# Optimization experiments

Hardware: AMD Instinct MI355X
Metric: run time of the kernel (lower is better)

Reference implementation:

```python
import jax, jax.numpy as jnp
import numpy as np

ROUTING_ITERS = 3
EPS = 1e-8


def squash(x):
    # scale = ||x||^2 / (1 + ||x||^2); out = scale * x / (||x|| + eps)
    norm = jnp.linalg.norm(x, axis=-1, keepdims=True)
    scale = norm ** 2 / (1.0 + norm ** 2)
    return scale * x / (norm + EPS)


def setup_inputs() -> dict:
    key = jax.random.key(0)
    kx, kw = jax.random.split(key)
    B, R, C, IC, OC = 256, 1152, 10, 8, 16
    x = jax.random.normal(kx, (B, R, IC), dtype=jnp.float32)
    # learned prediction weights: [1, num_routes, num_capsules, in_ch, out_ch]
    weights = jax.random.normal(kw, (1, R, C, IC, OC), dtype=jnp.float32)
    return {"x": x, "weights": weights}


def reference(x, weights):
    # prediction vectors u_hat[b,r,c,o] = sum_i x[b,r,i] * W[r,c,i,o]
    u = jnp.einsum('bri,rcio->brco', x, weights[0])  # [B,R,C,OC]
    b = jnp.zeros(u.shape[:3], dtype=u.dtype)        # routing logits [B,R,C]
    v = jnp.zeros(u.shape[:1] + u.shape[2:], dtype=u.dtype)
    for _ in range(ROUTING_ITERS):
        c = jax.nn.softmax(b, axis=-1)               # coupling coeffs over capsules
        s = jnp.einsum('brc,brco->bco', c, u)        # weighted sum over routes
        v = squash(s)                                # [B,C,OC]
        b = b + jnp.einsum('brco,bco->brc', u, v)    # agreement update
    return v
```

## Files before the change

### kernel.cpp

```cpp
#include <hip/hip_runtime.h>
#include <cstdint>
#include <cstddef>

#define NB 256
#define NR 1152
#define NC 10
#define NI 8
#define NO 16
#define NSPLIT 6
#define RSPL 192

static __device__ __forceinline__ uint32_t bf16_pack2(float lo, float hi) {
    uint32_t vl = __float_as_uint(lo);
    vl = vl + 0x7FFFu + ((vl >> 16) & 1u);
    uint32_t vh = __float_as_uint(hi);
    vh = vh + 0x7FFFu + ((vh >> 16) & 1u);
    return (vl >> 16) | (vh & 0xFFFF0000u);
}

__global__ __launch_bounds__(320, 2) void caps_u_kernel(
    const float* __restrict__ x, const float* __restrict__ W,
    uint32_t* __restrict__ u)
{
    const int t  = threadIdx.x;
    const int c  = t >> 5;
    const int rl = (t & 31) >> 2;
    const int oq = t & 3;
    const int rc = blockIdx.x >> 4;
    const int bg = blockIdx.x & 15;
    const int b0 = bg * 16;
    const int r  = rc * 8 + rl;

    __shared__ float xs[16][8][8];

    if (t < 256) {
        const int bi = t >> 4, rem = t & 15;
        const int rr = rem >> 1, hf = rem & 1;
        *(float4*)&xs[bi][rr][hf * 4] =
            *(const float4*)(x + ((size_t)(b0 + bi) * NR + rc * 8 + rr) * 8 + hf * 4);
    }

    const float* wb = W + ((size_t)r * NC + c) * (NI * NO) + oq * 4;
    float4 wf[8];
#pragma unroll
    for (int i = 0; i < 8; ++i) wf[i] = *(const float4*)(wb + i * NO);

    __syncthreads();

    for (int bi = 0; bi < 16; ++bi) {
        float xr[8];
#pragma unroll
        for (int i = 0; i < 8; ++i) xr[i] = xs[bi][rl][i];
        float ax = 0.f, ay = 0.f, az = 0.f, aw = 0.f;
#pragma unroll
        for (int i = 0; i < 8; ++i) {
            const float xv = xr[i];
            ax = fmaf(xv, wf[i].x, ax); ay = fmaf(xv, wf[i].y, ay);
            az = fmaf(xv, wf[i].z, az); aw = fmaf(xv, wf[i].w, aw);
        }
        uint2 s;
        s.x = bf16_pack2(ax, ay);
        s.y = bf16_pack2(az, aw);
        *(uint2*)(u + (((size_t)(b0 + bi) * NC + c) * NR + r) * 8 + oq * 2) = s;
    }
}

__global__ __launch_bounds__(256, 2) void caps_pass_kernel(
    const uint32_t* __restrict__ u, const float* __restrict__ vsum,
    float* __restrict__ part, const int mode)
{
    const int b  = blockIdx.x / NSPLIT;
    const int sp = blockIdx.x % NSPLIT;
    const int t  = threadIdx.x;
    const int oq = t & 3;
    const int rl = t >> 2;

    __shared__ float vss[160];
    __shared__ float sred[4][160];

    if (mode != 0 && t < 160) vss[t] = vsum[(size_t)b * 160 + t];
    __syncthreads();

    float acc[10][4];
#pragma unroll
    for (int c = 0; c < 10; ++c)
#pragma unroll
        for (int j = 0; j < 4; ++j) acc[c][j] = 0.f;

    const uint2* ub = (const uint2*)u + (size_t)b * NC * NR * 4 + oq;

    for (int k = 0; k < 3; ++k) {
        const int r = sp * RSPL + k * 64 + rl;
        uint2 q[10];
#pragma unroll
        for (int c = 0; c < 10; ++c) q[c] = ub[((size_t)c * NR + r) * 4];

        if (mode != 0) {
            float lg[10];
#pragma unroll
            for (int c = 0; c < 10; ++c) {
                const float4 vq = *(const float4*)&vss[c * 16 + oq * 4];
                float d = __uint_as_float(q[c].x << 16) * vq.x;
                d = fmaf(__uint_as_float(q[c].x & 0xFFFF0000u), vq.y, d);
                d = fmaf(__uint_as_float(q[c].y << 16),         vq.z, d);
                d = fmaf(__uint_as_float(q[c].y & 0xFFFF0000u), vq.w, d);
                lg[c] = d;
            }
#pragma unroll
            for (int c = 0; c < 10; ++c) {
                lg[c] += __shfl_xor(lg[c], 1);
                lg[c] += __shfl_xor(lg[c], 2);
            }
            float m = lg[0];
#pragma unroll
            for (int c = 1; c < 10; ++c) m = fmaxf(m, lg[c]);
            float wgt[10], ssum = 0.f;
#pragma unroll
            for (int c = 0; c < 10; ++c) { wgt[c] = __expf(lg[c] - m); ssum += wgt[c]; }
            const float inv = 1.f / ssum;
#pragma unroll
            for (int c = 0; c < 10; ++c) {
                const float wv = wgt[c] * inv;
                acc[c][0] = fmaf(wv, __uint_as_float(q[c].x << 16),         acc[c][0]);
                acc[c][1] = fmaf(wv, __uint_as_float(q[c].x & 0xFFFF0000u), acc[c][1]);
                acc[c][2] = fmaf(wv, __uint_as_float(q[c].y << 16),         acc[c][2]);
                acc[c][3] = fmaf(wv, __uint_as_float(q[c].y & 0xFFFF0000u), acc[c][3]);
            }
        } else {
#pragma unroll
            for (int c = 0; c < 10; ++c) {
                acc[c][0] += __uint_as_float(q[c].x << 16);
                acc[c][1] += __uint_as_float(q[c].x & 0xFFFF0000u);
                acc[c][2] += __uint_as_float(q[c].y << 16);
                acc[c][3] += __uint_as_float(q[c].y & 0xFFFF0000u);
            }
        }
    }

#pragma unroll
    for (int off = 4; off <= 32; off <<= 1)
#pragma unroll
        for (int c = 0; c < 10; ++c)
#pragma unroll
            for (int j = 0; j < 4; ++j) acc[c][j] += __shfl_xor(acc[c][j], off);

    const int wv = t >> 6;
    if ((t & 63) < 4) {
#pragma unroll
        for (int c = 0; c < 10; ++c)
#pragma unroll
            for (int j = 0; j < 4; ++j)
                sred[wv][c * 16 + oq * 4 + j] = acc[c][j];
    }
    __syncthreads();

    if (t < 160) {
        float s = sred[0][t] + sred[1][t] + sred[2][t] + sred[3][t];
        if (mode == 0) s *= 0.1f;
        part[((size_t)sp * NB + b) * 160 + t] = s;
    }
}

__global__ __launch_bounds__(192) void caps_reduce_kernel(
    const float* __restrict__ part, float* __restrict__ vsum,
    float* __restrict__ out, const int mode)
{
    const int b = blockIdx.x;
    const int t = threadIdx.x;
    if (t >= 160) return;
    float s = 0.f;
#pragma unroll
    for (int sp = 0; sp < NSPLIT; ++sp)
        s += part[((size_t)sp * NB + b) * 160 + t];
    float n2 = s * s;
    n2 += __shfl_xor(n2, 1);
    n2 += __shfl_xor(n2, 2);
    n2 += __shfl_xor(n2, 4);
    n2 += __shfl_xor(n2, 8);
    const float nrm   = sqrtf(n2);
    const float scale = n2 / (1.f + n2) / (nrm + 1e-8f);
    const float v = scale * s;
    if (mode == 0)      vsum[(size_t)b * 160 + t] = v;
    else if (mode == 1) vsum[(size_t)b * 160 + t] += v;
    else                out[(size_t)b * 160 + t] = v;
}

extern "C" void kernel_launch(void* const* d_in, const int* in_sizes, int n_in,
                              void* d_out, int out_size, void* d_ws, size_t ws_size,
                              hipStream_t stream) {
    const float* x = (const float*)d_in[0];
    const float* W = (const float*)d_in[1];
    float* out = (float*)d_out;

    uint8_t*  ws  = (uint8_t*)d_ws;
    uint32_t* u   = (uint32_t*)ws;
    float*    prt = (float*)(ws + 94371840u);
    float*    vsm = (float*)(ws + 94371840u + 983040u);

    caps_u_kernel     <<<2304, 320, 0, stream>>>(x, W, u);
    caps_pass_kernel  <<<NB * NSPLIT, 256, 0, stream>>>(u, vsm, prt, 0);
    caps_reduce_kernel<<<NB, 192, 0, stream>>>(prt, vsm, nullptr, 0);
    caps_pass_kernel  <<<NB * NSPLIT, 256, 0, stream>>>(u, vsm, prt, 1);
    caps_reduce_kernel<<<NB, 192, 0, stream>>>(prt, vsm, nullptr, 1);
    caps_pass_kernel  <<<NB * NSPLIT, 256, 0, stream>>>(u, vsm, prt, 1);
    caps_reduce_kernel<<<NB, 192, 0, stream>>>(prt, nullptr, out, 2);
}
```

Measured before the change: 159.4 us.

## Compute first routing pass from fp32 x and W instead of rereading u

Adds a separate kernel that recomputes the prediction vectors from x and W and reduces them across routes within each block, writing per-route-chunk partial sums. A dedicated reduce kernel turns these into the first squash output. This replaces the first full read of the bf16 u tensor, and the first pass now uses exact fp32 rather than bf16. The routing pass kernels now use a finer route split (18 splits of 64 routes, one route per thread), trading more blocks and a larger partial-sum buffer for higher parallelism. The cost is an extra read of W and a recompute of the einsum, plus a 23 MB partial buffer that the reduce kernel must read.

```diff
diff --git a/kernel.cpp b/kernel.cpp
--- a/kernel.cpp
+++ b/kernel.cpp
@@ -7,8 +7,9 @@
 #define NC 10
 #define NI 8
 #define NO 16
-#define NSPLIT 6
-#define RSPL 192
+#define NSPLIT 18
+#define RSPL 64
+#define NRC 144
 
 static __device__ __forceinline__ uint32_t bf16_pack2(float lo, float hi) {
     uint32_t vl = __float_as_uint(lo);
@@ -65,76 +66,136 @@
     }
 }
 
+__global__ __launch_bounds__(320, 2) void caps_s1_kernel(
+    const float* __restrict__ x, const float* __restrict__ W,
+    float* __restrict__ part1)
+{
+    const int t  = threadIdx.x;
+    const int c  = t >> 5;
+    const int rl = (t & 31) >> 2;
+    const int oq = t & 3;
+    const int rc = blockIdx.x >> 4;
+    const int bg = blockIdx.x & 15;
+    const int b0 = bg * 16;
+    const int r  = rc * 8 + rl;
+
+    __shared__ float xs[16][8][8];
+
+    if (t < 256) {
+        const int bi = t >> 4, rem = t & 15;
+        const int rr = rem >> 1, hf = rem & 1;
+        *(float4*)&xs[bi][rr][hf * 4] =
+            *(const float4*)(x + ((size_t)(b0 + bi) * NR + rc * 8 + rr) * 8 + hf * 4);
+    }
+
+    const float* wb = W + ((size_t)r * NC + c) * (NI * NO) + oq * 4;
+    float4 wf[8];
+#pragma unroll
+    for (int i = 0; i < 8; ++i) wf[i] = *(const float4*)(wb + i * NO);
+
+    __syncthreads();
+
+    for (int bi = 0; bi < 16; ++bi) {
+        float xr[8];
+#pragma unroll
+        for (int i = 0; i < 8; ++i) xr[i] = xs[bi][rl][i];
+        float a[4] = {0.f, 0.f, 0.f, 0.f};
+#pragma unroll
+        for (int i = 0; i < 8; ++i) {
+            const float xv = xr[i];
+            a[0] = fmaf(xv, wf[i].x, a[0]); a[1] = fmaf(xv, wf[i].y, a[1]);
+            a[2] = fmaf(xv, wf[i].z, a[2]); a[3] = fmaf(xv, wf[i].w, a[3]);
+        }
+#pragma unroll
+        for (int off = 4; off <= 16; off <<= 1)
+#pragma unroll
+            for (int j = 0; j < 4; ++j) a[j] += __shfl_xor(a[j], off);
+        if ((t & 28) == 0) {
+            *(float4*)(part1 + ((size_t)rc * NB + b0 + bi) * 160 + c * 16 + oq * 4)
+                = *(float4*)a;
+        }
+    }
+}
+
+__global__ __launch_bounds__(192) void caps_s1_reduce_kernel(
+    const float* __restrict__ part1, float* __restrict__ vsum)
+{
+    const int b = blockIdx.x;
+    const int t = threadIdx.x;
+    if (t >= 160) return;
+    float s0 = 0.f, s1 = 0.f, s2 = 0.f, s3 = 0.f;
+    const float* p = part1 + (size_t)b * 160 + t;
+#pragma unroll 4
+    for (int g = 0; g < NRC; g += 4) {
+        s0 += p[(size_t)(g + 0) * NB * 160];
+        s1 += p[(size_t)(g + 1) * NB * 160];
+        s2 += p[(size_t)(g + 2) * NB * 160];
+        s3 += p[(size_t)(g + 3) * NB * 160];
+    }
+    const float s = 0.1f * ((s0 + s1) + (s2 + s3));
+    float n2 = s * s;
+    n2 += __shfl_xor(n2, 1);
+    n2 += __shfl_xor(n2, 2);
+    n2 += __shfl_xor(n2, 4);
+    n2 += __shfl_xor(n2, 8);
+    const float nrm   = sqrtf(n2);
+    const float scale = n2 / (1.f + n2) / (nrm + 1e-8f);
+    vsum[(size_t)b * 160 + t] = scale * s;
+}
+
 __global__ __launch_bounds__(256, 2) void caps_pass_kernel(
     const uint32_t* __restrict__ u, const float* __restrict__ vsum,
-    float* __restrict__ part, const int mode)
+    float* __restrict__ part2)
 {
     const int b  = blockIdx.x / NSPLIT;
     const int sp = blockIdx.x % NSPLIT;
     const int t  = threadIdx.x;
     const int oq = t & 3;
     const int rl = t >> 2;
+    const int r  = sp * RSPL + rl;
 
     __shared__ float vss[160];
     __shared__ float sred[4][160];
 
-    if (mode != 0 && t < 160) vss[t] = vsum[(size_t)b * 160 + t];
-    __syncthreads();
+    if (t < 160) vss[t] = vsum[(size_t)b * 160 + t];
+    __syncthreads();
+
+    const uint2* ub = (const uint2*)u + (size_t)b * NC * NR * 4 + oq;
+    uint2 q[10];
+#pragma unroll
+    for (int c = 0; c < 10; ++c) q[c] = ub[((size_t)c * NR + r) * 4];
+
+    float lg[10];
+#pragma unroll
+    for (int c = 0; c < 10; ++c) {
+        const float4 vq = *(const float4*)&vss[c * 16 + oq * 4];
+        float d = __uint_as_float(q[c].x << 16) * vq.x;
+        d = fmaf(__uint_as_float(q[c].x & 0xFFFF0000u), vq.y, d);
+        d = fmaf(__uint_as_float(q[c].y << 16),         vq.z, d);
+        d = fmaf(__uint_as_float(q[c].y & 0xFFFF0000u), vq.w, d);
+        lg[c] = d;
+    }
+#pragma unroll
+    for (int c = 0; c < 10; ++c) {
+        lg[c] += __shfl_xor(lg[c], 1);
+        lg[c] += __shfl_xor(lg[c], 2);
+    }
+    float m = lg[0];
+#pragma unroll
+    for (int c = 1; c < 10; ++c) m = fmaxf(m, lg[c]);
+    float wgt[10], ssum = 0.f;
+#pragma unroll
+    for (int c = 0; c < 10; ++c) { wgt[c] = __expf(lg[c] - m); ssum += wgt[c]; }
+    const float inv = 1.f / ssum;
 
     float acc[10][4];
 #pragma unroll
-    for (int c = 0; c < 10; ++c)
-#pragma unroll
-        for (int j = 0; j < 4; ++j) acc[c][j] = 0.f;
-
-    const uint2* ub = (const uint2*)u + (size_t)b * NC * NR * 4 + oq;
-
-    for (int k = 0; k < 3; ++k) {
-        const int r = sp * RSPL + k * 64 + rl;
-        uint2 q[10];
-#pragma unroll
-        for (int c = 0; c < 10; ++c) q[c] = ub[((size_t)c * NR + r) * 4];
-
-        if (mode != 0) {
-            float lg[10];
-#pragma unroll
-            for (int c = 0; c < 10; ++c) {
-                const float4 vq = *(const float4*)&vss[c * 16 + oq * 4];
-                float d = __uint_as_float(q[c].x << 16) * vq.x;
-                d = fmaf(__uint_as_float(q[c].x & 0xFFFF0000u), vq.y, d);
-                d = fmaf(__uint_as_float(q[c].y << 16),         vq.z, d);
-                d = fmaf(__uint_as_float(q[c].y & 0xFFFF0000u), vq.w, d);
-                lg[c] = d;
-            }
-#pragma unroll
-            for (int c = 0; c < 10; ++c) {
-                lg[c] += __shfl_xor(lg[c], 1);
-                lg[c] += __shfl_xor(lg[c], 2);
-            }
-            float m = lg[0];
-#pragma unroll
-            for (int c = 1; c < 10; ++c) m = fmaxf(m, lg[c]);
-            float wgt[10], ssum = 0.f;
-#pragma unroll
-            for (int c = 0; c < 10; ++c) { wgt[c] = __expf(lg[c] - m); ssum += wgt[c]; }
-            const float inv = 1.f / ssum;
-#pragma unroll
-            for (int c = 0; c < 10; ++c) {
-                const float wv = wgt[c] * inv;
-                acc[c][0] = fmaf(wv, __uint_as_float(q[c].x << 16),         acc[c][0]);
-                acc[c][1] = fmaf(wv, __uint_as_float(q[c].x & 0xFFFF0000u), acc[c][1]);
-                acc[c][2] = fmaf(wv, __uint_as_float(q[c].y << 16),         acc[c][2]);
-                acc[c][3] = fmaf(wv, __uint_as_float(q[c].y & 0xFFFF0000u), acc[c][3]);
-            }
-        } else {
-#pragma unroll
-            for (int c = 0; c < 10; ++c) {
-                acc[c][0] += __uint_as_float(q[c].x << 16);
-                acc[c][1] += __uint_as_float(q[c].x & 0xFFFF0000u);
-                acc[c][2] += __uint_as_float(q[c].y << 16);
-                acc[c][3] += __uint_as_float(q[c].y & 0xFFFF0000u);
-            }
-        }
+    for (int c = 0; c < 10; ++c) {
+        const float wv = wgt[c] * inv;
+        acc[c][0] = wv * __uint_as_float(q[c].x << 16);
+        acc[c][1] = wv * __uint_as_float(q[c].x & 0xFFFF0000u);
+        acc[c][2] = wv * __uint_as_float(q[c].y << 16);
+        acc[c][3] = wv * __uint_as_float(q[c].y & 0xFFFF0000u);
     }
 
 #pragma unroll
@@ -155,14 +216,13 @@
     __syncthreads();
 
     if (t < 160) {
-        float s = sred[0][t] + sred[1][t] + sred[2][t] + sred[3][t];
-        if (mode == 0) s *= 0.1f;
-        part[((size_t)sp * NB + b) * 160 + t] = s;
+        part2[((size_t)sp * NB + b) * 160 + t]
+            = sred[0][t] + sred[1][t] + sred[2][t] + sred[3][t];
     }
 }
 
 __global__ __launch_bounds__(192) void caps_reduce_kernel(
-    const float* __restrict__ part, float* __restrict__ vsum,
+    const float* __restrict__ part2, float* __restrict__ vsum,
     float* __restrict__ out, const int mode)
 {
     const int b = blockIdx.x;
@@ -171,7 +231,7 @@
     float s = 0.f;
 #pragma unroll
     for (int sp = 0; sp < NSPLIT; ++sp)
-        s += part[((size_t)sp * NB + b) * 160 + t];
+        s += part2[((size_t)sp * NB + b) * 160 + t];
     float n2 = s * s;
     n2 += __shfl_xor(n2, 1);
     n2 += __shfl_xor(n2, 2);
@@ -180,9 +240,8 @@
     const float nrm   = sqrtf(n2);
     const float scale = n2 / (1.f + n2) / (nrm + 1e-8f);
     const float v = scale * s;
-    if (mode == 0)      vsum[(size_t)b * 160 + t] = v;
-    else if (mode == 1) vsum[(size_t)b * 160 + t] += v;
-    else                out[(size_t)b * 160 + t] = v;
+    if (mode == 1) vsum[(size_t)b * 160 + t] += v;
+    else           out[(size_t)b * 160 + t] = v;
 }
 
 extern "C" void kernel_launch(void* const* d_in, const int* in_sizes, int n_in,
@@ -192,16 +251,17 @@
     const float* W = (const float*)d_in[1];
     float* out = (float*)d_out;
 
-    uint8_t*  ws  = (uint8_t*)d_ws;
-    uint32_t* u   = (uint32_t*)ws;
-    float*    prt = (float*)(ws + 94371840u);
-    float*    vsm = (float*)(ws + 94371840u + 983040u);
-
-    caps_u_kernel     <<<2304, 320, 0, stream>>>(x, W, u);
-    caps_pass_kernel  <<<NB * NSPLIT, 256, 0, stream>>>(u, vsm, prt, 0);
-    caps_reduce_kernel<<<NB, 192, 0, stream>>>(prt, vsm, nullptr, 0);
-    caps_pass_kernel  <<<NB * NSPLIT, 256, 0, stream>>>(u, vsm, prt, 1);
-    caps_reduce_kernel<<<NB, 192, 0, stream>>>(prt, vsm, nullptr, 1);
-    caps_pass_kernel  <<<NB * NSPLIT, 256, 0, stream>>>(u, vsm, prt, 1);
-    caps_reduce_kernel<<<NB, 192, 0, stream>>>(prt, nullptr, out, 2);
-}
+    uint8_t*  ws   = (uint8_t*)d_ws;
+    uint32_t* u    = (uint32_t*)ws;
+    float*    prt1 = (float*)(ws + 94371840u);
+    float*    prt2 = (float*)(ws + 94371840u + 23592960u);
+    float*    vsm  = (float*)(ws + 94371840u + 23592960u + 2949120u);
+
+    caps_u_kernel        <<<2304, 320, 0, stream>>>(x, W, u);
+    caps_s1_kernel       <<<2304, 320, 0, stream>>>(x, W, prt1);
+    caps_s1_reduce_kernel<<<NB, 192, 0, stream>>>(prt1, vsm);
+    caps_pass_kernel     <<<NB * NSPLIT, 256, 0, stream>>>(u, vsm, prt2);
+    caps_reduce_kernel   <<<NB, 192, 0, stream>>>(prt2, vsm, nullptr, 1);
+    caps_pass_kernel     <<<NB * NSPLIT, 256, 0, stream>>>(u, vsm, prt2);
+    caps_reduce_kernel   <<<NB, 192, 0, stream>>>(prt2, nullptr, out, 2);
+}
```

Result: slower. 227.4 us (+42.7%).

## Split routing passes finer, preload all u loads, shorten shuffle reduction

Applied to the files above, without the earlier changes.

The route dimension is now split 9 ways instead of 6, giving more blocks. Each thread issues both halves of its u loads up front so more memory requests are in flight, and the pass kernel's launch bound is raised to 4 blocks per CU. The cross-lane shuffle reduction stops at offset 8, and the rest of the sum goes through a larger shared-memory table, trading shuffles for LDS traffic. The u kernel reads x from LDS as float4 and drops its occupancy hint; the partial buffer grows and the vsum offset moves to match.

```diff
diff --git a/kernel.cpp b/kernel.cpp
--- a/kernel.cpp
+++ b/kernel.cpp
@@ -7,8 +7,8 @@
 #define NC 10
 #define NI 8
 #define NO 16
-#define NSPLIT 6
-#define RSPL 192
+#define NSPLIT 9
+#define RSPL 128
 
 static __device__ __forceinline__ uint32_t bf16_pack2(float lo, float hi) {
     uint32_t vl = __float_as_uint(lo);
@@ -18,7 +18,7 @@
     return (vl >> 16) | (vh & 0xFFFF0000u);
 }
 
-__global__ __launch_bounds__(320, 2) void caps_u_kernel(
+__global__ __launch_bounds__(320) void caps_u_kernel(
     const float* __restrict__ x, const float* __restrict__ W,
     uint32_t* __restrict__ u)
 {
@@ -48,9 +48,10 @@
     __syncthreads();
 
     for (int bi = 0; bi < 16; ++bi) {
-        float xr[8];
-#pragma unroll
-        for (int i = 0; i < 8; ++i) xr[i] = xs[bi][rl][i];
+        const float4 xv4a = *(const float4*)&xs[bi][rl][0];
+        const float4 xv4b = *(const float4*)&xs[bi][rl][4];
+        const float xr[8] = {xv4a.x, xv4a.y, xv4a.z, xv4a.w,
+                             xv4b.x, xv4b.y, xv4b.z, xv4b.w};
         float ax = 0.f, ay = 0.f, az = 0.f, aw = 0.f;
 #pragma unroll
         for (int i = 0; i < 8; ++i) {
@@ -65,7 +66,7 @@
     }
 }
 
-__global__ __launch_bounds__(256, 2) void caps_pass_kernel(
+__global__ __launch_bounds__(256, 4) void caps_pass_kernel(
     const uint32_t* __restrict__ u, const float* __restrict__ vsum,
     float* __restrict__ part, const int mode)
 {
@@ -74,36 +75,39 @@
     const int t  = threadIdx.x;
     const int oq = t & 3;
     const int rl = t >> 2;
+    const int r0 = sp * RSPL + rl;
 
     __shared__ float vss[160];
-    __shared__ float sred[4][160];
+    __shared__ float sred[16][164];
 
     if (mode != 0 && t < 160) vss[t] = vsum[(size_t)b * 160 + t];
     __syncthreads();
 
+    const uint2* ub = (const uint2*)u + (size_t)b * NC * NR * 4 + oq;
+
+    uint2 q[2][10];
+#pragma unroll
+    for (int c = 0; c < 10; ++c) q[0][c] = ub[((size_t)c * NR + r0) * 4];
+#pragma unroll
+    for (int c = 0; c < 10; ++c) q[1][c] = ub[((size_t)c * NR + r0 + 64) * 4];
+
     float acc[10][4];
 #pragma unroll
     for (int c = 0; c < 10; ++c)
 #pragma unroll
         for (int j = 0; j < 4; ++j) acc[c][j] = 0.f;
 
-    const uint2* ub = (const uint2*)u + (size_t)b * NC * NR * 4 + oq;
-
-    for (int k = 0; k < 3; ++k) {
-        const int r = sp * RSPL + k * 64 + rl;
-        uint2 q[10];
-#pragma unroll
-        for (int c = 0; c < 10; ++c) q[c] = ub[((size_t)c * NR + r) * 4];
-
+#pragma unroll
+    for (int h = 0; h < 2; ++h) {
         if (mode != 0) {
             float lg[10];
 #pragma unroll
             for (int c = 0; c < 10; ++c) {
                 const float4 vq = *(const float4*)&vss[c * 16 + oq * 4];
-                float d = __uint_as_float(q[c].x << 16) * vq.x;
-                d = fmaf(__uint_as_float(q[c].x & 0xFFFF0000u), vq.y, d);
-                d = fmaf(__uint_as_float(q[c].y << 16),         vq.z, d);
-                d = fmaf(__uint_as_float(q[c].y & 0xFFFF0000u), vq.w, d);
+                float d = __uint_as_float(q[h][c].x << 16) * vq.x;
+                d = fmaf(__uint_as_float(q[h][c].x & 0xFFFF0000u), vq.y, d);
+                d = fmaf(__uint_as_float(q[h][c].y << 16),         vq.z, d);
+                d = fmaf(__uint_as_float(q[h][c].y & 0xFFFF0000u), vq.w, d);
                 lg[c] = d;
             }
 #pragma unroll
@@ -121,41 +125,45 @@
 #pragma unroll
             for (int c = 0; c < 10; ++c) {
                 const float wv = wgt[c] * inv;
-                acc[c][0] = fmaf(wv, __uint_as_float(q[c].x << 16),         acc[c][0]);
-                acc[c][1] = fmaf(wv, __uint_as_float(q[c].x & 0xFFFF0000u), acc[c][1]);
-                acc[c][2] = fmaf(wv, __uint_as_float(q[c].y << 16),         acc[c][2]);
-                acc[c][3] = fmaf(wv, __uint_as_float(q[c].y & 0xFFFF0000u), acc[c][3]);
+                acc[c][0] = fmaf(wv, __uint_as_float(q[h][c].x << 16),         acc[c][0]);
+                acc[c][1] = fmaf(wv, __uint_as_float(q[h][c].x & 0xFFFF0000u), acc[c][1]);
+                acc[c][2] = fmaf(wv, __uint_as_float(q[h][c].y << 16),         acc[c][2]);
+                acc[c][3] = fmaf(wv, __uint_as_float(q[h][c].y & 0xFFFF0000u), acc[c][3]);
             }
         } else {
 #pragma unroll
             for (int c = 0; c < 10; ++c) {
-                acc[c][0] += __uint_as_float(q[c].x << 16);
-                acc[c][1] += __uint_as_float(q[c].x & 0xFFFF0000u);
-                acc[c][2] += __uint_as_float(q[c].y << 16);
-                acc[c][3] += __uint_as_float(q[c].y & 0xFFFF0000u);
+                acc[c][0] += __uint_as_float(q[h][c].x << 16);
+                acc[c][1] += __uint_as_float(q[h][c].x & 0xFFFF0000u);
+                acc[c][2] += __uint_as_float(q[h][c].y << 16);
+                acc[c][3] += __uint_as_float(q[h][c].y & 0xFFFF0000u);
             }
         }
     }
 
 #pragma unroll
-    for (int off = 4; off <= 32; off <<= 1)
+    for (int off = 4; off <= 8; off <<= 1)
 #pragma unroll
         for (int c = 0; c < 10; ++c)
 #pragma unroll
             for (int j = 0; j < 4; ++j) acc[c][j] += __shfl_xor(acc[c][j], off);
 
-    const int wv = t >> 6;
-    if ((t & 63) < 4) {
+    const int lane = t & 63;
+    const int wv   = t >> 6;
+    const int g    = lane >> 4;
+    if (((lane >> 2) & 3) == 0) {
 #pragma unroll
         for (int c = 0; c < 10; ++c)
 #pragma unroll
             for (int j = 0; j < 4; ++j)
-                sred[wv][c * 16 + oq * 4 + j] = acc[c][j];
+                sred[wv * 4 + g][c * 16 + oq * 4 + j] = acc[c][j];
     }
     __syncthreads();
 
     if (t < 160) {
-        float s = sred[0][t] + sred[1][t] + sred[2][t] + sred[3][t];
+        float s = 0.f;
+#pragma unroll
+        for (int w = 0; w < 16; ++w) s += sred[w][t];
         if (mode == 0) s *= 0.1f;
         part[((size_t)sp * NB + b) * 160 + t] = s;
     }
@@ -195,7 +203,7 @@
     uint8_t*  ws  = (uint8_t*)d_ws;
     uint32_t* u   = (uint32_t*)ws;
     float*    prt = (float*)(ws + 94371840u);
-    float*    vsm = (float*)(ws + 94371840u + 983040u);
+    float*    vsm = (float*)(ws + 94371840u + 1474560u);
 
     caps_u_kernel     <<<2304, 320, 0, stream>>>(x, W, u);
     caps_pass_kernel  <<<NB * NSPLIT, 256, 0, stream>>>(u, vsm, prt, 0);
```

Measured after the change: 199.8 us. +25.4%, slower.

## Widen per-thread work to 8 outputs with 16-byte loads and halve route splits

Applied to the files above, without the earlier changes.

Both the prediction kernel and the routing pass kernel now give each thread 8 output channels instead of 4. Stores and loads of the bf16 u tensor become 16-byte vectors, and the prediction kernel handles 16 routes per block. The pass kernel uses 3 route splits of 384 instead of 6 of 192, so it writes fewer partials and sums them in a 32-row shared-memory reduction. The aim is fewer, wider memory transactions on the bandwidth-bound u reads and writes. The cost is higher register pressure and fewer blocks in the pass kernel, which may reduce occupancy.

```diff
diff --git a/kernel.cpp b/kernel.cpp
--- a/kernel.cpp
+++ b/kernel.cpp
@@ -7,8 +7,8 @@
 #define NC 10
 #define NI 8
 #define NO 16
-#define NSPLIT 6
-#define RSPL 192
+#define NSPLIT 3
+#define RSPL 384
 
 static __device__ __forceinline__ uint32_t bf16_pack2(float lo, float hi) {
     uint32_t vl = __float_as_uint(lo);
@@ -24,44 +24,51 @@
 {
     const int t  = threadIdx.x;
     const int c  = t >> 5;
-    const int rl = (t & 31) >> 2;
-    const int oq = t & 3;
+    const int rl = (t & 31) >> 1;
+    const int oh = t & 1;
     const int rc = blockIdx.x >> 4;
     const int bg = blockIdx.x & 15;
     const int b0 = bg * 16;
-    const int r  = rc * 8 + rl;
-
-    __shared__ float xs[16][8][8];
-
-    if (t < 256) {
-        const int bi = t >> 4, rem = t & 15;
+    const int r  = rc * 16 + rl;
+
+    __shared__ float xs[16][16][12];
+
+    for (int k = t; k < 512; k += 320) {
+        const int bi = k >> 5, rem = k & 31;
         const int rr = rem >> 1, hf = rem & 1;
         *(float4*)&xs[bi][rr][hf * 4] =
-            *(const float4*)(x + ((size_t)(b0 + bi) * NR + rc * 8 + rr) * 8 + hf * 4);
-    }
-
-    const float* wb = W + ((size_t)r * NC + c) * (NI * NO) + oq * 4;
-    float4 wf[8];
-#pragma unroll
-    for (int i = 0; i < 8; ++i) wf[i] = *(const float4*)(wb + i * NO);
-
+            *(const float4*)(x + ((size_t)(b0 + bi) * NR + rc * 16 + rr) * 8 + hf * 4);
+    }
+
+    const float* wb = W + ((size_t)r * NC + c) * (NI * NO) + oh * 8;
+    float4 wf[16];
+#pragma unroll
+    for (int i = 0; i < 8; ++i) {
+        wf[i * 2 + 0] = *(const float4*)(wb + i * NO);
+        wf[i * 2 + 1] = *(const float4*)(wb + i * NO + 4);
+    }
     __syncthreads();
 
     for (int bi = 0; bi < 16; ++bi) {
-        float xr[8];
-#pragma unroll
-        for (int i = 0; i < 8; ++i) xr[i] = xs[bi][rl][i];
-        float ax = 0.f, ay = 0.f, az = 0.f, aw = 0.f;
+        const float4 xa = *(const float4*)&xs[bi][rl][0];
+        const float4 xb = *(const float4*)&xs[bi][rl][4];
+        const float xr[8] = {xa.x, xa.y, xa.z, xa.w, xb.x, xb.y, xb.z, xb.w};
+        float a[8];
+#pragma unroll
+        for (int j = 0; j < 8; ++j) a[j] = 0.f;
 #pragma unroll
         for (int i = 0; i < 8; ++i) {
             const float xv = xr[i];
-            ax = fmaf(xv, wf[i].x, ax); ay = fmaf(xv, wf[i].y, ay);
-            az = fmaf(xv, wf[i].z, az); aw = fmaf(xv, wf[i].w, aw);
-        }
-        uint2 s;
-        s.x = bf16_pack2(ax, ay);
-        s.y = bf16_pack2(az, aw);
-        *(uint2*)(u + (((size_t)(b0 + bi) * NC + c) * NR + r) * 8 + oq * 2) = s;
+            const float4 w0 = wf[i * 2 + 0], w1 = wf[i * 2 + 1];
+            a[0] = fmaf(xv, w0.x, a[0]); a[1] = fmaf(xv, w0.y, a[1]);
+            a[2] = fmaf(xv, w0.z, a[2]); a[3] = fmaf(xv, w0.w, a[3]);
+            a[4] = fmaf(xv, w1.x, a[4]); a[5] = fmaf(xv, w1.y, a[5]);
+            a[6] = fmaf(xv, w1.z, a[6]); a[7] = fmaf(xv, w1.w, a[7]);
+        }
+        uint4 s;
+        s.x = bf16_pack2(a[0], a[1]); s.y = bf16_pack2(a[2], a[3]);
+        s.z = bf16_pack2(a[4], a[5]); s.w = bf16_pack2(a[6], a[7]);
+        *(uint4*)(u + (((size_t)(b0 + bi) * NC + c) * NR + r) * 8 + oh * 4) = s;
     }
 }
 
@@ -72,90 +79,101 @@
     const int b  = blockIdx.x / NSPLIT;
     const int sp = blockIdx.x % NSPLIT;
     const int t  = threadIdx.x;
-    const int oq = t & 3;
-    const int rl = t >> 2;
+    const int oh = t & 1;
+    const int rl = t >> 1;
 
     __shared__ float vss[160];
-    __shared__ float sred[4][160];
+    __shared__ float sred[32][164];
 
     if (mode != 0 && t < 160) vss[t] = vsum[(size_t)b * 160 + t];
     __syncthreads();
 
-    float acc[10][4];
+    float acc[10][8];
 #pragma unroll
     for (int c = 0; c < 10; ++c)
 #pragma unroll
-        for (int j = 0; j < 4; ++j) acc[c][j] = 0.f;
-
-    const uint2* ub = (const uint2*)u + (size_t)b * NC * NR * 4 + oq;
+        for (int j = 0; j < 8; ++j) acc[c][j] = 0.f;
+
+    const uint4* ub = (const uint4*)u + (size_t)b * NC * NR * 2 + oh;
 
     for (int k = 0; k < 3; ++k) {
-        const int r = sp * RSPL + k * 64 + rl;
-        uint2 q[10];
-#pragma unroll
-        for (int c = 0; c < 10; ++c) q[c] = ub[((size_t)c * NR + r) * 4];
-
+        const int r = sp * RSPL + k * 128 + rl;
+        uint4 q[10];
+#pragma unroll
+        for (int c = 0; c < 10; ++c) q[c] = ub[((size_t)c * NR + r) * 2];
+
+        float wgt[10];
         if (mode != 0) {
             float lg[10];
 #pragma unroll
             for (int c = 0; c < 10; ++c) {
-                const float4 vq = *(const float4*)&vss[c * 16 + oq * 4];
-                float d = __uint_as_float(q[c].x << 16) * vq.x;
-                d = fmaf(__uint_as_float(q[c].x & 0xFFFF0000u), vq.y, d);
-                d = fmaf(__uint_as_float(q[c].y << 16),         vq.z, d);
-                d = fmaf(__uint_as_float(q[c].y & 0xFFFF0000u), vq.w, d);
+                const float4 v0 = *(const float4*)&vss[c * 16 + oh * 8];
+                const float4 v1 = *(const float4*)&vss[c * 16 + oh * 8 + 4];
+                float d;
+                d = __uint_as_float(q[c].x << 16)                 * v0.x;
+                d = fmaf(__uint_as_float(q[c].x & 0xFFFF0000u), v0.y, d);
+                d = fmaf(__uint_as_float(q[c].y << 16),         v0.z, d);
+                d = fmaf(__uint_as_float(q[c].y & 0xFFFF0000u), v0.w, d);
+                d = fmaf(__uint_as_float(q[c].z << 16),         v1.x, d);
+                d = fmaf(__uint_as_float(q[c].z & 0xFFFF0000u), v1.y, d);
+                d = fmaf(__uint_as_float(q[c].w << 16),         v1.z, d);
+                d = fmaf(__uint_as_float(q[c].w & 0xFFFF0000u), v1.w, d);
                 lg[c] = d;
             }
 #pragma unroll
-            for (int c = 0; c < 10; ++c) {
+            for (int c = 0; c < 10; ++c)
                 lg[c] += __shfl_xor(lg[c], 1);
-                lg[c] += __shfl_xor(lg[c], 2);
-            }
             float m = lg[0];
 #pragma unroll
             for (int c = 1; c < 10; ++c) m = fmaxf(m, lg[c]);
-            float wgt[10], ssum = 0.f;
+            float ssum = 0.f;
 #pragma unroll
             for (int c = 0; c < 10; ++c) { wgt[c] = __expf(lg[c] - m); ssum += wgt[c]; }
             const float inv = 1.f / ssum;
 #pragma unroll
-            for (int c = 0; c < 10; ++c) {
-                const float wv = wgt[c] * inv;
-                acc[c][0] = fmaf(wv, __uint_as_float(q[c].x << 16),         acc[c][0]);
-                acc[c][1] = fmaf(wv, __uint_as_float(q[c].x & 0xFFFF0000u), acc[c][1]);
-                acc[c][2] = fmaf(wv, __uint_as_float(q[c].y << 16),         acc[c][2]);
-                acc[c][3] = fmaf(wv, __uint_as_float(q[c].y & 0xFFFF0000u), acc[c][3]);
-            }
+            for (int c = 0; c < 10; ++c) wgt[c] *= inv;
         } else {
 #pragma unroll
-            for (int c = 0; c < 10; ++c) {
-                acc[c][0] += __uint_as_float(q[c].x << 16);
-                acc[c][1] += __uint_as_float(q[c].x & 0xFFFF0000u);
-                acc[c][2] += __uint_as_float(q[c].y << 16);
-                acc[c][3] += __uint_as_float(q[c].y & 0xFFFF0000u);
-            }
-        }
-    }
-
-#pragma unroll
-    for (int off = 4; off <= 32; off <<= 1)
+            for (int c = 0; c < 10; ++c) wgt[c] = 1.f;
+        }
+#pragma unroll
+        for (int c = 0; c < 10; ++c) {
+            const float wv = wgt[c];
+            acc[c][0] = fmaf(wv, __uint_as_float(q[c].x << 16),         acc[c][0]);
+            acc[c][1] = fmaf(wv, __uint_as_float(q[c].x & 0xFFFF0000u), acc[c][1]);
+            acc[c][2] = fmaf(wv, __uint_as_float(q[c].y << 16),         acc[c][2]);
+            acc[c][3] = fmaf(wv, __uint_as_float(q[c].y & 0xFFFF0000u), acc[c][3]);
+            acc[c][4] = fmaf(wv, __uint_as_float(q[c].z << 16),         acc[c][4]);
+            acc[c][5] = fmaf(wv, __uint_as_float(q[c].z & 0xFFFF0000u), acc[c][5]);
+            acc[c][6] = fmaf(wv, __uint_as_float(q[c].w << 16),         acc[c][6]);
+            acc[c][7] = fmaf(wv, __uint_as_float(q[c].w & 0xFFFF0000u), acc[c][7]);
+        }
+    }
+
+#pragma unroll
+    for (int off = 2; off <= 4; off <<= 1)
 #pragma unroll
         for (int c = 0; c < 10; ++c)
 #pragma unroll
-            for (int j = 0; j < 4; ++j) acc[c][j] += __shfl_xor(acc[c][j], off);
-
-    const int wv = t >> 6;
-    if ((t & 63) < 4) {
-#pragma unroll
-        for (int c = 0; c < 10; ++c)
-#pragma unroll
-            for (int j = 0; j < 4; ++j)
-                sred[wv][c * 16 + oq * 4 + j] = acc[c][j];
+            for (int j = 0; j < 8; ++j) acc[c][j] += __shfl_xor(acc[c][j], off);
+
+    const int lane = t & 63;
+    const int wv   = t >> 6;
+    if (((lane >> 1) & 3) == 0) {
+        const int g   = lane >> 3;
+        const int row = wv * 8 + g;
+#pragma unroll
+        for (int c = 0; c < 10; ++c) {
+            *(float4*)&sred[row][c * 16 + oh * 8]     = *(float4*)&acc[c][0];
+            *(float4*)&sred[row][c * 16 + oh * 8 + 4] = *(float4*)&acc[c][4];
+        }
     }
     __syncthreads();
 
     if (t < 160) {
-        float s = sred[0][t] + sred[1][t] + sred[2][t] + sred[3][t];
+        float s = 0.f;
+#pragma unroll
+        for (int w = 0; w < 32; ++w) s += sred[w][t];
         if (mode == 0) s *= 0.1f;
         part[((size_t)sp * NB + b) * 160 + t] = s;
     }
@@ -195,9 +213,9 @@
     uint8_t*  ws  = (uint8_t*)d_ws;
     uint32_t* u   = (uint32_t*)ws;
     float*    prt = (float*)(ws + 94371840u);
-    float*    vsm = (float*)(ws + 94371840u + 983040u);
-
-    caps_u_kernel     <<<2304, 320, 0, stream>>>(x, W, u);
+    float*    vsm = (float*)(ws + 94371840u + 491520u);
+
+    caps_u_kernel     <<<1152, 320, 0, stream>>>(x, W, u);
     caps_pass_kernel  <<<NB * NSPLIT, 256, 0, stream>>>(u, vsm, prt, 0);
     caps_reduce_kernel<<<NB, 192, 0, stream>>>(prt, vsm, nullptr, 0);
     caps_pass_kernel  <<<NB * NSPLIT, 256, 0, stream>>>(u, vsm, prt, 1);
```

Result: slower. 170.0 us (+6.7%).
